# Optimization experiments

Measured on AMD Instinct MI355X. Metric: run time of the kernel, lower is better.

Reference implementation:

```python
import jax, jax.numpy as jnp
import numpy as np

TAU = 0.1
EPS = 1e-8  # torch CosineSimilarity eps


def _neg_indices(B):
    # static (numpy) column indices of the non-masked (negative) entries per row
    N = 2 * B
    mask = ~(np.eye(N, dtype=bool)
             | np.eye(N, k=B, dtype=bool)
             | np.eye(N, k=-B, dtype=bool))
    return np.where(mask)[1].reshape(N, N - 2)  # [2B, 2B-2]


def setup_inputs() -> dict:
    key = jax.random.key(0)
    k1, k2 = jax.random.split(key)
    zis = jax.random.normal(k1, (4096, 128), dtype=jnp.float32)
    zjs = jax.random.normal(k2, (4096, 128), dtype=jnp.float32)
    return {"zis": zis, "zjs": zjs}


def reference(zis, zjs):
    B = zis.shape[0]
    N = 2 * B
    reps = jnp.concatenate([zjs, zis], axis=0)  # [2B, D]
    # cosine similarity via normalize + GEMM
    norm = jnp.linalg.norm(reps, axis=-1, keepdims=True)
    rn = reps / jnp.maximum(norm, EPS)
    sim = rn @ rn.T  # [2B, 2B]

    l_pos = jnp.diagonal(sim, offset=B)   # [B]
    r_pos = jnp.diagonal(sim, offset=-B)  # [B]
    positives = jnp.concatenate([l_pos, r_pos])[:, None]  # [2B, 1]

    neg_idx = jnp.asarray(_neg_indices(B))  # static [2B, 2B-2]
    negatives = jnp.take_along_axis(sim, neg_idx, axis=1)  # [2B, 2B-2]

    logits = jnp.concatenate([positives, negatives], axis=1) / TAU  # [2B, 2B-1]
    logp = jax.nn.log_softmax(logits, axis=-1)
    # labels are all zeros; CrossEntropyLoss(reduction='sum')
    CE = -jnp.sum(logp[:, 0])
    # pt = mean over full [2B, 2B-1] of onehot * softmax = sum softmax[:,0] / (2B*(2B-1))
    pt = jnp.sum(jnp.exp(logp[:, 0])) / (N * (N - 1))
    epsilon = float(B)
    loss = CE / N + epsilon * (1.0 / B - pt)
    return loss
```

## Files before the change

### kernel.cpp

```cpp
#include <hip/hip_runtime.h>
#include <hip/hip_bf16.h>

#define BSZ 4096
#define NSZ 8192
#define DD  128
#define TILE 128
#define GROUPS 8
#define TPB 8

typedef __attribute__((ext_vector_type(8))) short bf16x8;
typedef __attribute__((ext_vector_type(4))) float f32x4;

typedef __attribute__((address_space(3))) unsigned int lds_u32;
typedef const __attribute__((address_space(1))) unsigned int glb_u32;

__global__ __launch_bounds__(256)
void norm_kernel(const float* __restrict__ zis,
                 const float* __restrict__ zjs,
                 __hip_bfloat16* __restrict__ rn) {
    const int row  = blockIdx.x * 4 + (threadIdx.x >> 6);
    const int lane = threadIdx.x & 63;
    const float* src = (row < BSZ) ? (zjs + (size_t)row * DD)
                                   : (zis + (size_t)(row - BSZ) * DD);
    float2 v = *(const float2*)(src + lane * 2);
    float ss = v.x * v.x + v.y * v.y;
    #pragma unroll
    for (int off = 32; off; off >>= 1) ss += __shfl_xor(ss, off);
    float inv = 1.0f / fmaxf(sqrtf(ss), 1e-8f);
    __hip_bfloat16 a = __float2bfloat16(v.x * inv);
    __hip_bfloat16 b = __float2bfloat16(v.y * inv);
    ushort2 pk;
    pk.x = *(const ushort*)&a;
    pk.y = *(const ushort*)&b;
    *(ushort2*)(rn + (size_t)row * DD + lane * 2) = pk;
}

__global__ __launch_bounds__(512, 4)
void sim_lse_kernel(const __hip_bfloat16* __restrict__ rn,
                    float* __restrict__ partials,
                    float* __restrict__ pos) {
    __shared__ ushort As[TILE * DD];
    __shared__ ushort Bs[TILE * DD];

    const int g   = blockIdx.x;
    const int bi  = blockIdx.y;
    const int tid = threadIdx.x;
    const int wid  = tid >> 6;
    const int lane = tid & 63;
    const int l15  = lane & 15;
    const int kg   = lane >> 4;
    const int wm   = wid >> 1;
    const int wn   = wid & 1;

    {
        const char* ga = (const char*)rn + (size_t)bi * TILE * 256;
        const char* gb = (const char*)rn + (size_t)(g * TPB) * TILE * 256;
        #pragma unroll
        for (int j = 0; j < 4; ++j) {
            int cs  = (wid * 4 + j) * 64 + lane;
            int gsc = cs ^ ((cs >> 4) & 7);
            __builtin_amdgcn_global_load_lds((glb_u32*)(ga + (size_t)gsc * 16),
                                             (lds_u32*)(As + (wid * 4 + j) * 512),
                                             16, 0, 0);
            __builtin_amdgcn_global_load_lds((glb_u32*)(gb + (size_t)gsc * 16),
                                             (lds_u32*)(Bs + (wid * 4 + j) * 512),
                                             16, 0, 0);
        }
    }
    __syncthreads();

    float rsum[2][4] = {};
    const int bjp = (bi + 32) & 63;
    const int nfd = (wm & 1) * 2;
    const bool wdiag = (wn == (wm >> 1));
    const char* Ab = (const char*)As;
    const char* Bb = (const char*)Bs;

    for (int t = 0; t < TPB; ++t) {
        const int bj = g * TPB + t;

        f32x4 acc[2][4] = {};
        #pragma unroll
        for (int kk = 0; kk < 4; ++kk) {
            const int kb = kk * 64 + kg * 16;
            bf16x8 afr[2];
            #pragma unroll
            for (int mf = 0; mf < 2; ++mf) {
                int rR = wm * 32 + mf * 16 + l15;
                int o = rR * 256 + kb;
                afr[mf] = *(const bf16x8*)(Ab + (o ^ ((rR & 7) << 4)));
            }
            bf16x8 bfr[4];
            #pragma unroll
            for (int nf = 0; nf < 4; ++nf) {
                int cR = wn * 64 + nf * 16 + l15;
                int o = cR * 256 + kb;
                bfr[nf] = *(const bf16x8*)(Bb + (o ^ ((cR & 7) << 4)));
            }
            #pragma unroll
            for (int mf = 0; mf < 2; ++mf)
                #pragma unroll
                for (int nf = 0; nf < 4; ++nf)
                    acc[mf][nf] = __builtin_amdgcn_mfma_f32_16x16x32_bf16(
                        afr[mf], bfr[nf], acc[mf][nf], 0, 0, 0);
        }

        const bool dglb = (bj == bi)  && wdiag;
        const bool pglb = (bj == bjp) && wdiag;
        #pragma unroll
        for (int mf = 0; mf < 2; ++mf) {
            #pragma unroll
            for (int nf = 0; nf < 4; ++nf) {
                #pragma unroll
                for (int reg = 0; reg < 4; ++reg) {
                    float s = acc[mf][nf][reg];
                    bool hit = (nf == nfd + mf) && (kg * 4 + reg == l15);
                    if (pglb && hit)
                        pos[bi * TILE + wm * 32 + mf * 16 + l15] = s;
                    float p = __expf(s * 10.0f);
                    if (dglb && hit) p = 0.0f;
                    rsum[mf][reg] += p;
                }
            }
        }

        __syncthreads();

        if (t + 1 < TPB) {
            const char* gb = (const char*)rn + (size_t)(bj + 1) * TILE * 256;
            #pragma unroll
            for (int j = 0; j < 4; ++j) {
                int cs  = (wid * 4 + j) * 64 + lane;
                int gsc = cs ^ ((cs >> 4) & 7);
                __builtin_amdgcn_global_load_lds((glb_u32*)(gb + (size_t)gsc * 16),
                                                 (lds_u32*)(Bs + (wid * 4 + j) * 512),
                                                 16, 0, 0);
            }
            __syncthreads();
        }
    }

    #pragma unroll
    for (int mf = 0; mf < 2; ++mf)
        #pragma unroll
        for (int reg = 0; reg < 4; ++reg) {
            float v = rsum[mf][reg];
            v += __shfl_xor(v, 1);
            v += __shfl_xor(v, 2);
            v += __shfl_xor(v, 4);
            v += __shfl_xor(v, 8);
            if (l15 == 0)
                partials[(size_t)(g * 2 + wn) * NSZ
                         + bi * TILE + wm * 32 + mf * 16 + kg * 4 + reg] = v;
        }
}

__global__ __launch_bounds__(1024)
void reduce_kernel(const float* __restrict__ partials,
                   const float* __restrict__ pos,
                   float* __restrict__ out) {
    int tid = threadIdx.x;
    int base = tid * 8;
    float se[8] = {0.f, 0.f, 0.f, 0.f, 0.f, 0.f, 0.f, 0.f};
    #pragma unroll
    for (int gr = 0; gr < 2 * GROUPS; ++gr) {
        const float* p = partials + (size_t)gr * NSZ + base;
        float4 a = *(const float4*)(p);
        float4 b = *(const float4*)(p + 4);
        se[0] += a.x; se[1] += a.y; se[2] += a.z; se[3] += a.w;
        se[4] += b.x; se[5] += b.y; se[6] += b.z; se[7] += b.w;
    }
    float ce = 0.f, pt = 0.f;
    #pragma unroll
    for (int h = 0; h < 2; ++h) {
        float4 p4 = *(const float4*)(pos + base + h * 4);
        const float* pp = (const float*)&p4;
        #pragma unroll
        for (int q = 0; q < 4; ++q) {
            float s = se[h * 4 + q];
            ce += __logf(s) - pp[q] * 10.0f;
            pt += __expf(pp[q] * 10.0f) / s;
        }
    }
    #pragma unroll
    for (int off = 32; off; off >>= 1) {
        ce += __shfl_xor(ce, off);
        pt += __shfl_xor(pt, off);
    }
    __shared__ float lce[16], lpt[16];
    if ((tid & 63) == 0) { lce[tid >> 6] = ce; lpt[tid >> 6] = pt; }
    __syncthreads();
    if (tid == 0) {
        float CE = 0.f, PT = 0.f;
        #pragma unroll
        for (int w = 0; w < 16; ++w) { CE += lce[w]; PT += lpt[w]; }
        float loss = CE / (float)NSZ + 1.0f
                   - PT * ((float)BSZ / ((float)NSZ * (float)(NSZ - 1)));
        out[0] = loss;
    }
}

extern "C" void kernel_launch(void* const* d_in, const int* in_sizes, int n_in,
                              void* d_out, int out_size, void* d_ws, size_t ws_size,
                              hipStream_t stream) {
    const float* zis = (const float*)d_in[0];
    const float* zjs = (const float*)d_in[1];
    float* out = (float*)d_out;

    char* ws = (char*)d_ws;
    __hip_bfloat16* rn = (__hip_bfloat16*)ws;
    float* partials = (float*)(ws + 2 * 1024 * 1024);
    float* pos      = (float*)(ws + 2 * 1024 * 1024 + 512 * 1024);

    norm_kernel<<<NSZ / 4, 256, 0, stream>>>(zis, zjs, rn);

    dim3 grid(GROUPS, 64);
    sim_lse_kernel<<<grid, 512, 0, stream>>>(rn, partials, pos);

    reduce_kernel<<<1, 1024, 0, stream>>>(partials, pos, out);
}
```

Before: 41.74 us.

## Enlarge A tile to 256 rows and double-buffer B tile loads

```diff
diff --git a/kernel.cpp b/kernel.cpp
--- a/kernel.cpp
+++ b/kernel.cpp
@@ -4,7 +4,6 @@
 #define BSZ 4096
 #define NSZ 8192
 #define DD  128
-#define TILE 128
 #define GROUPS 8
 #define TPB 8
 
@@ -35,12 +34,12 @@
     *(ushort2*)(rn + (size_t)row * DD + lane * 2) = pk;
 }
 
-__global__ __launch_bounds__(512, 4)
+__global__ __launch_bounds__(512) __attribute__((amdgpu_waves_per_eu(2, 2)))
 void sim_lse_kernel(const __hip_bfloat16* __restrict__ rn,
                     float* __restrict__ partials,
                     float* __restrict__ pos) {
-    __shared__ ushort As[TILE * DD];
-    __shared__ ushort Bs[TILE * DD];
+    __shared__ ushort As[256 * DD];
+    __shared__ ushort Bt[2][128 * DD];
 
     const int g   = blockIdx.x;
     const int bi  = blockIdx.y;
@@ -53,40 +52,57 @@
     const int wn   = wid & 1;
 
     {
-        const char* ga = (const char*)rn + (size_t)bi * TILE * 256;
-        const char* gb = (const char*)rn + (size_t)(g * TPB) * TILE * 256;
+        const char* ga = (const char*)rn + (size_t)bi * 256 * 256;
+        #pragma unroll
+        for (int j = 0; j < 8; ++j) {
+            int cs  = (wid * 8 + j) * 64 + lane;
+            int gsc = cs ^ ((cs >> 4) & 7);
+            __builtin_amdgcn_global_load_lds((glb_u32*)(ga + (size_t)gsc * 16),
+                                             (lds_u32*)(As + (wid * 8 + j) * 512),
+                                             16, 0, 0);
+        }
+        const char* gb = (const char*)rn + (size_t)(g * TPB) * 128 * 256;
         #pragma unroll
         for (int j = 0; j < 4; ++j) {
             int cs  = (wid * 4 + j) * 64 + lane;
             int gsc = cs ^ ((cs >> 4) & 7);
-            __builtin_amdgcn_global_load_lds((glb_u32*)(ga + (size_t)gsc * 16),
-                                             (lds_u32*)(As + (wid * 4 + j) * 512),
+            __builtin_amdgcn_global_load_lds((glb_u32*)(gb + (size_t)gsc * 16),
+                                             (lds_u32*)(&Bt[0][0] + (wid * 4 + j) * 512),
                                              16, 0, 0);
-            __builtin_amdgcn_global_load_lds((glb_u32*)(gb + (size_t)gsc * 16),
-                                             (lds_u32*)(Bs + (wid * 4 + j) * 512),
-                                             16, 0, 0);
         }
     }
     __syncthreads();
 
-    float rsum[2][4] = {};
-    const int bjp = (bi + 32) & 63;
-    const int nfd = (wm & 1) * 2;
-    const bool wdiag = (wn == (wm >> 1));
+    float rsum[4][4] = {};
+    const int ru = bi * 4 + wm;
+    const int pu = (ru + 64) & 127;
     const char* Ab = (const char*)As;
-    const char* Bb = (const char*)Bs;
 
     for (int t = 0; t < TPB; ++t) {
         const int bj = g * TPB + t;
 
-        f32x4 acc[2][4] = {};
+        if (t + 1 < TPB) {
+            const char* gb = (const char*)rn + (size_t)(bj + 1) * 128 * 256;
+            ushort* dst = &Bt[(t + 1) & 1][0];
+            #pragma unroll
+            for (int j = 0; j < 4; ++j) {
+                int cs  = (wid * 4 + j) * 64 + lane;
+                int gsc = cs ^ ((cs >> 4) & 7);
+                __builtin_amdgcn_global_load_lds((glb_u32*)(gb + (size_t)gsc * 16),
+                                                 (lds_u32*)(dst + (wid * 4 + j) * 512),
+                                                 16, 0, 0);
+            }
+        }
+
+        f32x4 acc[4][4] = {};
+        const char* Bb = (const char*)&Bt[t & 1][0];
         #pragma unroll
         for (int kk = 0; kk < 4; ++kk) {
             const int kb = kk * 64 + kg * 16;
-            bf16x8 afr[2];
-            #pragma unroll
-            for (int mf = 0; mf < 2; ++mf) {
-                int rR = wm * 32 + mf * 16 + l15;
+            bf16x8 afr[4];
+            #pragma unroll
+            for (int mf = 0; mf < 4; ++mf) {
+                int rR = wm * 64 + mf * 16 + l15;
                 int o = rR * 256 + kb;
                 afr[mf] = *(const bf16x8*)(Ab + (o ^ ((rR & 7) << 4)));
             }
@@ -98,25 +114,26 @@
                 bfr[nf] = *(const bf16x8*)(Bb + (o ^ ((cR & 7) << 4)));
             }
             #pragma unroll
-            for (int mf = 0; mf < 2; ++mf)
+            for (int mf = 0; mf < 4; ++mf)
                 #pragma unroll
                 for (int nf = 0; nf < 4; ++nf)
                     acc[mf][nf] = __builtin_amdgcn_mfma_f32_16x16x32_bf16(
                         afr[mf], bfr[nf], acc[mf][nf], 0, 0, 0);
         }
 
-        const bool dglb = (bj == bi)  && wdiag;
-        const bool pglb = (bj == bjp) && wdiag;
-        #pragma unroll
-        for (int mf = 0; mf < 2; ++mf) {
+        const int cu = bj * 2 + wn;
+        const bool dglb = (cu == ru);
+        const bool pglb = (cu == pu);
+        #pragma unroll
+        for (int mf = 0; mf < 4; ++mf) {
             #pragma unroll
             for (int nf = 0; nf < 4; ++nf) {
                 #pragma unroll
                 for (int reg = 0; reg < 4; ++reg) {
                     float s = acc[mf][nf][reg];
-                    bool hit = (nf == nfd + mf) && (kg * 4 + reg == l15);
+                    bool hit = (mf == nf) && (kg * 4 + reg == l15);
                     if (pglb && hit)
-                        pos[bi * TILE + wm * 32 + mf * 16 + l15] = s;
+                        pos[ru * 64 + mf * 16 + l15] = s;
                     float p = __expf(s * 10.0f);
                     if (dglb && hit) p = 0.0f;
                     rsum[mf][reg] += p;
@@ -125,23 +142,10 @@
         }
 
         __syncthreads();
-
-        if (t + 1 < TPB) {
-            const char* gb = (const char*)rn + (size_t)(bj + 1) * TILE * 256;
-            #pragma unroll
-            for (int j = 0; j < 4; ++j) {
-                int cs  = (wid * 4 + j) * 64 + lane;
-                int gsc = cs ^ ((cs >> 4) & 7);
-                __builtin_amdgcn_global_load_lds((glb_u32*)(gb + (size_t)gsc * 16),
-                                                 (lds_u32*)(Bs + (wid * 4 + j) * 512),
-                                                 16, 0, 0);
-            }
-            __syncthreads();
-        }
-    }
-
-    #pragma unroll
-    for (int mf = 0; mf < 2; ++mf)
+    }
+
+    #pragma unroll
+    for (int mf = 0; mf < 4; ++mf)
         #pragma unroll
         for (int reg = 0; reg < 4; ++reg) {
             float v = rsum[mf][reg];
@@ -151,7 +155,7 @@
             v += __shfl_xor(v, 8);
             if (l15 == 0)
                 partials[(size_t)(g * 2 + wn) * NSZ
-                         + bi * TILE + wm * 32 + mf * 16 + kg * 4 + reg] = v;
+                         + ru * 64 + mf * 16 + kg * 4 + reg] = v;
         }
 }
 
@@ -214,7 +218,7 @@
 
     norm_kernel<<<NSZ / 4, 256, 0, stream>>>(zis, zjs, rn);
 
-    dim3 grid(GROUPS, 64);
+    dim3 grid(GROUPS, 32);
     sim_lse_kernel<<<grid, 512, 0, stream>>>(rn, partials, pos);
 
     reduce_kernel<<<1, 1024, 0, stream>>>(partials, pos, out);
```

Measured after the change: 42.71 us. 2.3% more time.
